# Kernel tuning notes

Hardware: AMD Instinct MI355X
Metric: run time of the kernel (lower is better)

Reference implementation:

```python
import jax, jax.numpy as jnp
import numpy as np

N_NODES = 100000
N_EDGES = 1600000
D_FEAT = 32
EPS = 1e-12  # F.normalize clamp eps


def setup_inputs() -> dict:
    key = jax.random.key(0)
    k1, k2, k3 = jax.random.split(key, 3)
    feat = jax.random.normal(k1, (N_NODES, D_FEAT), dtype=jnp.float32)
    beta = jnp.ones((1,), dtype=jnp.float32)
    src = jax.random.randint(k2, (N_EDGES,), 0, N_NODES, dtype=jnp.int32)
    dst = jax.random.randint(k3, (N_EDGES,), 0, N_NODES, dtype=jnp.int32)
    return {"feat": feat, "beta": beta, "src": src, "dst": dst}


def reference(feat, beta, src, dst):
    N = feat.shape[0]
    # L2-normalize node features (torch.nn.functional.normalize semantics)
    norm = jnp.maximum(jnp.linalg.norm(feat, axis=-1, keepdims=True), EPS)
    norm_h = feat / norm
    # per-edge cosine similarity: u_dot_v
    cos = jnp.sum(norm_h[src] * norm_h[dst], axis=-1)  # [E]
    e = beta[0] * cos
    # edge softmax over incoming edges of each dst node
    m = jax.lax.stop_gradient(jax.ops.segment_max(e, dst, num_segments=N))
    m = jnp.where(jnp.isfinite(m), m, 0.0)  # nodes with no in-edges
    p = jnp.exp(e - m[dst])
    s = jax.ops.segment_sum(p, dst, num_segments=N)
    p = p / s[dst]
    # weighted message aggregation: u_mul_e -> sum
    out = jax.ops.segment_sum(feat[src] * p[:, None], dst, num_segments=N)
    return out
```

## Files before the change

kernel.cpp:

```cpp
#include <hip/hip_runtime.h>
#include <hip/hip_bf16.h>

#define D_FEAT 32
#define BUCKET_SHIFT 7
#define BUCKET_NODES 128
#define MAX_NB 1024
#define CHUNK_E 8192
#define REC_CHUNK 4096

typedef __attribute__((ext_vector_type(8))) unsigned short u16x8;
typedef __attribute__((ext_vector_type(8))) float f32x8;

static __device__ __forceinline__ unsigned short f2bf(float x) {
    unsigned int u = __float_as_uint(x);
    u += 0x7FFFu + ((u >> 16) & 1u);
    return (unsigned short)(u >> 16);
}
static __device__ __forceinline__ float bf2f(unsigned short b) {
    return __uint_as_float((unsigned int)b << 16);
}

__global__ __launch_bounds__(256) void prep_hist_kernel(
    const float* __restrict__ feat,
    unsigned short* __restrict__ nfb,
    float* __restrict__ inv_norm,
    const int* __restrict__ dst,
    int* __restrict__ chunk_hist,
    int n_nodes, int n_edges, int nb, int nchunk) {

    __shared__ int s_h[MAX_NB];
    int bid = blockIdx.x;
    int t = threadIdx.x;

    if (bid < nchunk) {
        for (int i = t; i < MAX_NB; i += 256) s_h[i] = 0;
        __syncthreads();
        int base = bid * CHUNK_E;
        int cnt = min(CHUNK_E, n_edges - base);
        int cnt4 = cnt >> 2;
        const int4* dst4 = reinterpret_cast<const int4*>(dst + base);
        for (int k = t; k < cnt4; k += 256) {
            int4 d4 = dst4[k];
            atomicAdd(&s_h[d4.x >> BUCKET_SHIFT], 1);
            atomicAdd(&s_h[d4.y >> BUCKET_SHIFT], 1);
            atomicAdd(&s_h[d4.z >> BUCKET_SHIFT], 1);
            atomicAdd(&s_h[d4.w >> BUCKET_SHIFT], 1);
        }
        for (int k = (cnt4 << 2) + t; k < cnt; k += 256)
            atomicAdd(&s_h[dst[base + k] >> BUCKET_SHIFT], 1);
        __syncthreads();
        for (int i = t; i < nb; i += 256)
            chunk_hist[(size_t)i * nchunk + bid] = s_h[i];
    } else {
        int g = (bid - nchunk) * 256 + t;
        int node = g >> 3;
        int lane = g & 7;
        if (node >= n_nodes) return;
        float4 v = reinterpret_cast<const float4*>(feat + (size_t)node * D_FEAT)[lane];
        float ss = v.x * v.x + v.y * v.y + v.z * v.z + v.w * v.w;
        #pragma unroll
        for (int m = 4; m; m >>= 1) ss += __shfl_xor(ss, m, 8);
        if (lane == 0) inv_norm[node] = 1.0f / fmaxf(sqrtf(ss), 1e-12f);
        ushort4 b;
        b.x = f2bf(v.x); b.y = f2bf(v.y); b.z = f2bf(v.z); b.w = f2bf(v.w);
        reinterpret_cast<ushort4*>(nfb + (size_t)node * D_FEAT)[lane] = b;
    }
}

__global__ void col_prefix_kernel(int* __restrict__ chunk_hist,
                                  int* __restrict__ total, int nchunk, int nb) {
    int wid  = (blockIdx.x * blockDim.x + threadIdx.x) >> 6;
    int lane = threadIdx.x & 63;
    if (wid >= nb) return;
    int* row = chunk_hist + (size_t)wid * nchunk;
    int run = 0;
    for (int base = 0; base < nchunk; base += 64) {
        int c = base + lane;
        int v = (c < nchunk) ? row[c] : 0;
        int incl = v;
        #pragma unroll
        for (int off = 1; off < 64; off <<= 1) {
            int n = __shfl_up(incl, off, 64);
            if (lane >= off) incl += n;
        }
        if (c < nchunk) row[c] = run + (incl - v);
        run += __shfl(incl, 63, 64);
    }
    if (lane == 0) total[wid] = run;
}

__global__ __launch_bounds__(256) void base_scan_kernel(const int* __restrict__ total,
                                                        int* __restrict__ bucket_base,
                                                        int nb, int n_edges) {
    __shared__ int s_sum[256];
    int t = threadIdx.x;
    int i0 = t * 4;
    int a[4];
    int tsum = 0;
    #pragma unroll
    for (int j = 0; j < 4; ++j) {
        a[j] = (i0 + j < nb) ? total[i0 + j] : 0;
        tsum += a[j];
    }
    s_sum[t] = tsum;
    __syncthreads();
    for (int off = 1; off < 256; off <<= 1) {
        int add = (t >= off) ? s_sum[t - off] : 0;
        __syncthreads();
        s_sum[t] += add;
        __syncthreads();
    }
    int run = s_sum[t] - tsum;
    #pragma unroll
    for (int j = 0; j < 4; ++j) {
        if (i0 + j < nb) bucket_base[i0 + j] = run;
        run += a[j];
    }
    if (t == 0) bucket_base[nb] = n_edges;
}

__global__ __launch_bounds__(256) void scatter_kernel(const int* __restrict__ src,
                                                      const int* __restrict__ dst,
                                                      const int* __restrict__ chunk_hist,
                                                      const int* __restrict__ bucket_base,
                                                      int* __restrict__ recs,
                                                      int n_edges, int nb, int nchunk) {
    __shared__ int s_cur[MAX_NB];
    __shared__ int s_off[MAX_NB + 1];
    __shared__ int s_gbase[MAX_NB];
    __shared__ int s_sum[256];
    __shared__ int s_rec[CHUNK_E];
    __shared__ unsigned short s_b[CHUNK_E];

    int c = blockIdx.x;
    int t = threadIdx.x;
    int base = c * CHUNK_E;
    int cnt = min(CHUNK_E, n_edges - base);
    int cnt4 = cnt >> 2;
    const int4* dst4 = reinterpret_cast<const int4*>(dst + base);
    const int4* src4 = reinterpret_cast<const int4*>(src + base);

    for (int i = t; i < MAX_NB; i += 256) s_cur[i] = 0;
    __syncthreads();
    for (int k = t; k < cnt4; k += 256) {
        int4 d4 = dst4[k];
        atomicAdd(&s_cur[d4.x >> BUCKET_SHIFT], 1);
        atomicAdd(&s_cur[d4.y >> BUCKET_SHIFT], 1);
        atomicAdd(&s_cur[d4.z >> BUCKET_SHIFT], 1);
        atomicAdd(&s_cur[d4.w >> BUCKET_SHIFT], 1);
    }
    for (int k = (cnt4 << 2) + t; k < cnt; k += 256)
        atomicAdd(&s_cur[dst[base + k] >> BUCKET_SHIFT], 1);
    __syncthreads();

    int i0 = t * 4;
    int a[4];
    int tsum = 0;
    #pragma unroll
    for (int j = 0; j < 4; ++j) { a[j] = s_cur[i0 + j]; tsum += a[j]; }
    s_sum[t] = tsum;
    __syncthreads();
    for (int off = 1; off < 256; off <<= 1) {
        int add = (t >= off) ? s_sum[t - off] : 0;
        __syncthreads();
        s_sum[t] += add;
        __syncthreads();
    }
    int run = s_sum[t] - tsum;
    #pragma unroll
    for (int j = 0; j < 4; ++j) { s_off[i0 + j] = run; run += a[j]; }
    if (t == 255) s_off[MAX_NB] = run;
    __syncthreads();
    for (int i = t; i < MAX_NB; i += 256) s_cur[i] = s_off[i];
    for (int i = t; i < nb; i += 256)
        s_gbase[i] = bucket_base[i] + chunk_hist[(size_t)i * nchunk + c];
    __syncthreads();

    for (int k = t; k < cnt4; k += 256) {
        int4 d4 = dst4[k];
        int4 s4 = src4[k];
        #pragma unroll
        for (int j = 0; j < 4; ++j) {
            int d = (j == 0) ? d4.x : (j == 1) ? d4.y : (j == 2) ? d4.z : d4.w;
            int s = (j == 0) ? s4.x : (j == 1) ? s4.y : (j == 2) ? s4.z : s4.w;
            int bb = d >> BUCKET_SHIFT;
            int lpos = atomicAdd(&s_cur[bb], 1);
            s_rec[lpos] = (s << BUCKET_SHIFT) | (d & (BUCKET_NODES - 1));
            s_b[lpos] = (unsigned short)bb;
        }
    }
    for (int k = (cnt4 << 2) + t; k < cnt; k += 256) {
        int d = dst[base + k];
        int s = src[base + k];
        int bb = d >> BUCKET_SHIFT;
        int lpos = atomicAdd(&s_cur[bb], 1);
        s_rec[lpos] = (s << BUCKET_SHIFT) | (d & (BUCKET_NODES - 1));
        s_b[lpos] = (unsigned short)bb;
    }
    __syncthreads();

    for (int i = t; i < cnt; i += 256) {
        int bb = s_b[i];
        recs[s_gbase[bb] + (i - s_off[bb])] = s_rec[i];
    }
}

__global__ __launch_bounds__(512) void bucket_aggregate_kernel(
    const unsigned short* __restrict__ nfb,
    const float* __restrict__ inv_norm,
    const int* __restrict__ bucket_base,
    const int* __restrict__ recs,
    const float* __restrict__ beta,
    float* __restrict__ out, int n_nodes) {

    __shared__ int s_rec[REC_CHUNK];
    __shared__ int s_hist[BUCKET_NODES];
    __shared__ int s_off[BUCKET_NODES + 1];

    int b = blockIdx.x;
    int node0 = b * BUCKET_NODES;
    int start = bucket_base[b];
    int end   = bucket_base[b + 1];
    int t = threadIdx.x;
    int group = t >> 2;
    int lane  = t & 3;
    float bscale = beta[0];

    int myv = node0 + group;
    f32x8 bn;
    f32x8 acc;
    float ssum = 0.f;
    #pragma unroll
    for (int j = 0; j < 8; ++j) { bn[j] = 0.f; acc[j] = 0.f; }
    if (myv < n_nodes) {
        u16x8 braw = reinterpret_cast<const u16x8*>(nfb + (size_t)myv * D_FEAT)[lane];
        float invv = inv_norm[myv];
        #pragma unroll
        for (int j = 0; j < 8; ++j) bn[j] = bf2f(braw[j]) * invv;
    }

    for (int cbase = start; cbase < end; cbase += REC_CHUNK) {
        int cnt = min(REC_CHUNK, end - cbase);

        if (t < BUCKET_NODES) s_hist[t] = 0;
        __syncthreads();
        for (int i = t; i < cnt; i += 512)
            atomicAdd(&s_hist[recs[cbase + i] & (BUCKET_NODES - 1)], 1);
        __syncthreads();

        if (t < 64) {
            int v0 = s_hist[2 * t];
            int v1 = s_hist[2 * t + 1];
            int pair = v0 + v1;
            int incl = pair;
            #pragma unroll
            for (int off = 1; off < 64; off <<= 1) {
                int n = __shfl_up(incl, off, 64);
                if (t >= off) incl += n;
            }
            int excl = incl - pair;
            s_off[2 * t]     = excl;
            s_off[2 * t + 1] = excl + v0;
            s_hist[2 * t]     = excl;
            s_hist[2 * t + 1] = excl + v0;
            if (t == 63) s_off[BUCKET_NODES] = incl;
        }
        __syncthreads();

        for (int i = t; i < cnt; i += 512) {
            int r = recs[cbase + i];
            int pos = atomicAdd(&s_hist[r & (BUCKET_NODES - 1)], 1);
            s_rec[pos] = r;
        }
        __syncthreads();

        {
            int rs = s_off[group];
            int re = s_off[group + 1];

            int u0 = 0; float invu0 = 0.f;
            u16x8 araw0;
            #pragma unroll
            for (int j = 0; j < 8; ++j) araw0[j] = 0;
            if (rs < re) {
                u0 = ((unsigned)s_rec[rs]) >> BUCKET_SHIFT;
                invu0 = inv_norm[u0];
                araw0 = reinterpret_cast<const u16x8*>(nfb + (size_t)u0 * D_FEAT)[lane];
            }
            for (int i = rs; i < re; ++i) {
                int u1 = 0; float invu1 = 0.f;
                u16x8 araw1;
                #pragma unroll
                for (int j = 0; j < 8; ++j) araw1[j] = 0;
                if (i + 1 < re) {
                    u1 = ((unsigned)s_rec[i + 1]) >> BUCKET_SHIFT;
                    invu1 = inv_norm[u1];
                    araw1 = reinterpret_cast<const u16x8*>(nfb + (size_t)u1 * D_FEAT)[lane];
                }
                f32x8 a;
                float d = 0.f;
                #pragma unroll
                for (int j = 0; j < 8; ++j) {
                    a[j] = bf2f(araw0[j]);
                    d = fmaf(a[j], bn[j], d);
                }
                d += __shfl_xor(d, 1, 4);
                d += __shfl_xor(d, 2, 4);
                float pe = __expf(bscale * d * invu0);
                #pragma unroll
                for (int j = 0; j < 8; ++j) acc[j] = fmaf(pe, a[j], acc[j]);
                ssum += pe;
                u0 = u1; invu0 = invu1; araw0 = araw1;
            }
        }
        __syncthreads();
    }

    if (myv < n_nodes) {
        float inv_s = (ssum > 0.f) ? (1.0f / ssum) : 0.0f;
        float* op = out + (size_t)myv * D_FEAT + lane * 8;
        reinterpret_cast<float4*>(op)[0] =
            make_float4(acc[0] * inv_s, acc[1] * inv_s, acc[2] * inv_s, acc[3] * inv_s);
        reinterpret_cast<float4*>(op)[1] =
            make_float4(acc[4] * inv_s, acc[5] * inv_s, acc[6] * inv_s, acc[7] * inv_s);
    }
}

__global__ void prep_kernel(const float* __restrict__ feat,
                            unsigned short* __restrict__ nfb,
                            float* __restrict__ inv_norm, int n_nodes) {
    int g = blockIdx.x * blockDim.x + threadIdx.x;
    int node = g >> 3;
    int lane = g & 7;
    if (node >= n_nodes) return;
    float4 v = reinterpret_cast<const float4*>(feat + (size_t)node * D_FEAT)[lane];
    float ss = v.x * v.x + v.y * v.y + v.z * v.z + v.w * v.w;
    #pragma unroll
    for (int m = 4; m; m >>= 1) ss += __shfl_xor(ss, m, 8);
    if (lane == 0) inv_norm[node] = 1.0f / fmaxf(sqrtf(ss), 1e-12f);
    ushort4 b;
    b.x = f2bf(v.x); b.y = f2bf(v.y); b.z = f2bf(v.z); b.w = f2bf(v.w);
    reinterpret_cast<ushort4*>(nfb + (size_t)node * D_FEAT)[lane] = b;
}

__global__ void link_packed_kernel(const int* __restrict__ src,
                                   const int* __restrict__ dst,
                                   int* __restrict__ head,
                                   int2* __restrict__ rec, int n_edges) {
    int stride = gridDim.x * blockDim.x;
    for (int e = blockIdx.x * blockDim.x + threadIdx.x; e < n_edges; e += stride) {
        int d = dst[e];
        int s = src[e];
        int old = atomicExch(&head[d], e);
        rec[e] = make_int2(old, s);
    }
}

__global__ void fused_chase_bf16_kernel(const unsigned short* __restrict__ nfb,
                                        const float* __restrict__ inv_norm,
                                        const int* __restrict__ head,
                                        const int2* __restrict__ rec,
                                        const float* __restrict__ beta,
                                        float* __restrict__ out, int n_nodes) {
    int g = blockIdx.x * blockDim.x + threadIdx.x;
    int node = g >> 2;
    int lane = g & 3;
    if (node >= n_nodes) return;

    float bscale = beta[0];
    float invv = inv_norm[node];
    u16x8 braw = reinterpret_cast<const u16x8*>(nfb + (size_t)node * D_FEAT)[lane];
    f32x8 bn;
    #pragma unroll
    for (int j = 0; j < 8; ++j) bn[j] = bf2f(braw[j]) * invv;

    f32x8 acc;
    #pragma unroll
    for (int j = 0; j < 8; ++j) acc[j] = 0.f;
    float ssum = 0.f;

    int e = head[node];
    while (e >= 0) {
        int2 r = rec[e];
        int en = r.x, u = r.y;
        float invu = inv_norm[u];
        u16x8 araw = reinterpret_cast<const u16x8*>(nfb + (size_t)u * D_FEAT)[lane];
        f32x8 a;
        float d = 0.f;
        #pragma unroll
        for (int j = 0; j < 8; ++j) {
            a[j] = bf2f(araw[j]);
            d = fmaf(a[j], bn[j], d);
        }
        d += __shfl_xor(d, 1, 4);
        d += __shfl_xor(d, 2, 4);
        float pe = __expf(bscale * d * invu);
        #pragma unroll
        for (int j = 0; j < 8; ++j) acc[j] = fmaf(pe, a[j], acc[j]);
        ssum += pe;
        e = en;
    }

    float inv_s = (ssum > 0.f) ? (1.0f / ssum) : 0.0f;
    float* op = out + (size_t)node * D_FEAT + lane * 8;
    reinterpret_cast<float4*>(op)[0] =
        make_float4(acc[0] * inv_s, acc[1] * inv_s, acc[2] * inv_s, acc[3] * inv_s);
    reinterpret_cast<float4*>(op)[1] =
        make_float4(acc[4] * inv_s, acc[5] * inv_s, acc[6] * inv_s, acc[7] * inv_s);
}

__global__ void node_invnorm_kernel(const float* __restrict__ feat,
                                    float* __restrict__ inv_norm, int n_nodes) {
    int g = blockIdx.x * blockDim.x + threadIdx.x;
    int node = g >> 3;
    int lane = g & 7;
    if (node >= n_nodes) return;
    float4 v = reinterpret_cast<const float4*>(feat + (size_t)node * D_FEAT)[lane];
    float ss = v.x * v.x + v.y * v.y + v.z * v.z + v.w * v.w;
    #pragma unroll
    for (int m = 4; m; m >>= 1) ss += __shfl_xor(ss, m, 8);
    if (lane == 0) inv_norm[node] = 1.0f / fmaxf(sqrtf(ss), 1e-12f);
}

__global__ void edge_p_kernel(const float* __restrict__ feat,
                              const float* __restrict__ inv_norm,
                              const int* __restrict__ src,
                              const int* __restrict__ dst,
                              const float* __restrict__ beta,
                              float* __restrict__ p, float* __restrict__ s,
                              int n_edges) {
    int g = blockIdx.x * blockDim.x + threadIdx.x;
    int e = g >> 3;
    int lane = g & 7;
    if (e >= n_edges) return;
    int u = src[e];
    int v = dst[e];
    float4 a = reinterpret_cast<const float4*>(feat + (size_t)u * D_FEAT)[lane];
    float4 b = reinterpret_cast<const float4*>(feat + (size_t)v * D_FEAT)[lane];
    float d = a.x * b.x;
    d = fmaf(a.y, b.y, d);
    d = fmaf(a.z, b.z, d);
    d = fmaf(a.w, b.w, d);
    #pragma unroll
    for (int m = 4; m; m >>= 1) d += __shfl_xor(d, m, 8);
    if (lane == 0) {
        float pe = __expf(beta[0] * d * inv_norm[u] * inv_norm[v]);
        p[e] = pe;
        atomicAdd(&s[v], pe);
    }
}

__global__ void aggregate_atomic_kernel(const float* __restrict__ feat,
                                        const int* __restrict__ src,
                                        const int* __restrict__ dst,
                                        const float* __restrict__ p,
                                        const float* __restrict__ s,
                                        float* __restrict__ out, int n_edges) {
    int g = blockIdx.x * blockDim.x + threadIdx.x;
    int e = g >> 5;
    int lane = g & 31;
    if (e >= n_edges) return;
    int u = src[e];
    int v = dst[e];
    float w = p[e] / s[v];
    atomicAdd(&out[(size_t)v * D_FEAT + lane], feat[(size_t)u * D_FEAT + lane] * w);
}

extern "C" void kernel_launch(void* const* d_in, const int* in_sizes, int n_in,
                              void* d_out, int out_size, void* d_ws, size_t ws_size,
                              hipStream_t stream) {
    const float* feat = (const float*)d_in[0];
    const float* beta = (const float*)d_in[1];
    const int*   src  = (const int*)d_in[2];
    const int*   dst  = (const int*)d_in[3];
    float* out = (float*)d_out;

    int n_nodes = in_sizes[0] / D_FEAT;
    int n_edges = in_sizes[2];
    int nb = (n_nodes + BUCKET_NODES - 1) / BUCKET_NODES;
    int nchunk = (n_edges + CHUNK_E - 1) / CHUNK_E;

    size_t nfb_bytes = (size_t)n_nodes * D_FEAT * 2;
    size_t need_sort = nfb_bytes +
                       ((size_t)n_nodes + (nb + 1) + MAX_NB +
                        (size_t)nb * nchunk + (size_t)n_edges) * 4;
    size_t need_ll = nfb_bytes + (size_t)n_nodes * 8 + (size_t)n_edges * 8;

    bool sort_ok = (ws_size >= need_sort) && (nb <= MAX_NB) &&
                   (n_nodes <= (1 << 24));

    if (sort_ok) {
        unsigned short* nfb = (unsigned short*)d_ws;
        float* inv_norm   = (float*)((char*)d_ws + nfb_bytes);
        int* bucket_base  = (int*)(inv_norm + n_nodes);
        int* total        = bucket_base + (nb + 1);
        int* chunk_hist   = total + MAX_NB;
        int* recs         = chunk_hist + (size_t)nb * nchunk;

        {
            int prep_blocks = (n_nodes * 8 + 255) / 256;
            prep_hist_kernel<<<nchunk + prep_blocks, 256, 0, stream>>>(
                feat, nfb, inv_norm, dst, chunk_hist, n_nodes, n_edges, nb, nchunk);
        }
        {
            int blocks = (nb + 3) / 4;
            col_prefix_kernel<<<blocks, 256, 0, stream>>>(chunk_hist, total, nchunk, nb);
        }
        base_scan_kernel<<<1, 256, 0, stream>>>(total, bucket_base, nb, n_edges);
        scatter_kernel<<<nchunk, 256, 0, stream>>>(src, dst, chunk_hist, bucket_base,
                                                   recs, n_edges, nb, nchunk);
        bucket_aggregate_kernel<<<nb, 512, 0, stream>>>(
            nfb, inv_norm, bucket_base, recs, beta, out, n_nodes);
    } else if (ws_size >= need_ll) {
        unsigned short* nfb = (unsigned short*)d_ws;
        float* inv_norm = (float*)((char*)d_ws + nfb_bytes);
        int*   head     = (int*)(inv_norm + n_nodes);
        int2*  rec      = (int2*)(head + n_nodes);

        hipMemsetAsync(head, 0xFF, (size_t)n_nodes * sizeof(int), stream);
        {
            int tt = n_nodes * 8;
            prep_kernel<<<(tt + 255) / 256, 256, 0, stream>>>(feat, nfb, inv_norm, n_nodes);
        }
        link_packed_kernel<<<2048, 256, 0, stream>>>(src, dst, head, rec, n_edges);
        {
            int tt = n_nodes * 4;
            fused_chase_bf16_kernel<<<(tt + 255) / 256, 256, 0, stream>>>(
                nfb, inv_norm, head, rec, beta, out, n_nodes);
        }
    } else {
        float* inv_norm = (float*)d_ws;
        float* s_sum    = inv_norm + n_nodes;
        float* p        = s_sum + n_nodes;

        hipMemsetAsync(s_sum, 0, (size_t)n_nodes * sizeof(float), stream);
        hipMemsetAsync(out, 0, (size_t)out_size * sizeof(float), stream);

        {
            int tt = n_nodes * 8;
            node_invnorm_kernel<<<(tt + 255) / 256, 256, 0, stream>>>(feat, inv_norm, n_nodes);
        }
        {
            long long tt = (long long)n_edges * 8;
            edge_p_kernel<<<(int)((tt + 255) / 256), 256, 0, stream>>>(
                feat, inv_norm, src, dst, beta, p, s_sum, n_edges);
        }
        {
            long long tt = (long long)n_edges * 32;
            aggregate_atomic_kernel<<<(int)((tt + 255) / 256), 256, 0, stream>>>(
                feat, src, dst, p, s_sum, out, n_edges);
        }
    }
}
```

Baseline: 73.56 us.

## Split each aggregation bucket across two blocks and two edge streams per node

The aggregate kernel now launches two blocks per 128-node bucket, each owning 64 nodes, and assigns two 4-lane groups per node that walk alternating incoming edges, then combines their partial sums through shared memory. Records are loaded into registers once per chunk instead of being read twice from global memory. The scatter kernel is widened to 512 threads per block. The aim is more parallelism and shorter per-node serial chains in the edge loop. The cost is that each bucket's record list is now read and filtered by two blocks, and there is an extra shared-memory reduction.

```diff
diff --git a/kernel.cpp b/kernel.cpp
--- a/kernel.cpp
+++ b/kernel.cpp
@@ -119,7 +119,7 @@
     if (t == 0) bucket_base[nb] = n_edges;
 }
 
-__global__ __launch_bounds__(256) void scatter_kernel(const int* __restrict__ src,
+__global__ __launch_bounds__(512) void scatter_kernel(const int* __restrict__ src,
                                                       const int* __restrict__ dst,
                                                       const int* __restrict__ chunk_hist,
                                                       const int* __restrict__ bucket_base,
@@ -128,7 +128,7 @@
     __shared__ int s_cur[MAX_NB];
     __shared__ int s_off[MAX_NB + 1];
     __shared__ int s_gbase[MAX_NB];
-    __shared__ int s_sum[256];
+    __shared__ int s_sum[512];
     __shared__ int s_rec[CHUNK_E];
     __shared__ unsigned short s_b[CHUNK_E];
 
@@ -140,43 +140,41 @@
     const int4* dst4 = reinterpret_cast<const int4*>(dst + base);
     const int4* src4 = reinterpret_cast<const int4*>(src + base);
 
-    for (int i = t; i < MAX_NB; i += 256) s_cur[i] = 0;
-    __syncthreads();
-    for (int k = t; k < cnt4; k += 256) {
+    for (int i = t; i < MAX_NB; i += 512) s_cur[i] = 0;
+    __syncthreads();
+    for (int k = t; k < cnt4; k += 512) {
         int4 d4 = dst4[k];
         atomicAdd(&s_cur[d4.x >> BUCKET_SHIFT], 1);
         atomicAdd(&s_cur[d4.y >> BUCKET_SHIFT], 1);
         atomicAdd(&s_cur[d4.z >> BUCKET_SHIFT], 1);
         atomicAdd(&s_cur[d4.w >> BUCKET_SHIFT], 1);
     }
-    for (int k = (cnt4 << 2) + t; k < cnt; k += 256)
+    for (int k = (cnt4 << 2) + t; k < cnt; k += 512)
         atomicAdd(&s_cur[dst[base + k] >> BUCKET_SHIFT], 1);
     __syncthreads();
 
-    int i0 = t * 4;
-    int a[4];
-    int tsum = 0;
-    #pragma unroll
-    for (int j = 0; j < 4; ++j) { a[j] = s_cur[i0 + j]; tsum += a[j]; }
+    int i0 = t * 2;
+    int a0 = s_cur[i0], a1 = s_cur[i0 + 1];
+    int tsum = a0 + a1;
     s_sum[t] = tsum;
     __syncthreads();
-    for (int off = 1; off < 256; off <<= 1) {
+    for (int off = 1; off < 512; off <<= 1) {
         int add = (t >= off) ? s_sum[t - off] : 0;
         __syncthreads();
         s_sum[t] += add;
         __syncthreads();
     }
     int run = s_sum[t] - tsum;
-    #pragma unroll
-    for (int j = 0; j < 4; ++j) { s_off[i0 + j] = run; run += a[j]; }
-    if (t == 255) s_off[MAX_NB] = run;
-    __syncthreads();
-    for (int i = t; i < MAX_NB; i += 256) s_cur[i] = s_off[i];
-    for (int i = t; i < nb; i += 256)
+    s_off[i0] = run;
+    s_off[i0 + 1] = run + a0;
+    if (t == 511) s_off[MAX_NB] = run + tsum;
+    __syncthreads();
+    for (int i = t; i < MAX_NB; i += 512) s_cur[i] = s_off[i];
+    for (int i = t; i < nb; i += 512)
         s_gbase[i] = bucket_base[i] + chunk_hist[(size_t)i * nchunk + c];
     __syncthreads();
 
-    for (int k = t; k < cnt4; k += 256) {
+    for (int k = t; k < cnt4; k += 512) {
         int4 d4 = dst4[k];
         int4 s4 = src4[k];
         #pragma unroll
@@ -189,7 +187,7 @@
             s_b[lpos] = (unsigned short)bb;
         }
     }
-    for (int k = (cnt4 << 2) + t; k < cnt; k += 256) {
+    for (int k = (cnt4 << 2) + t; k < cnt; k += 512) {
         int d = dst[base + k];
         int s = src[base + k];
         int bb = d >> BUCKET_SHIFT;
@@ -199,7 +197,7 @@
     }
     __syncthreads();
 
-    for (int i = t; i < cnt; i += 256) {
+    for (int i = t; i < cnt; i += 512) {
         int bb = s_b[i];
         recs[s_gbase[bb] + (i - s_off[bb])] = s_rec[i];
     }
@@ -214,19 +212,24 @@
     float* __restrict__ out, int n_nodes) {
 
     __shared__ int s_rec[REC_CHUNK];
-    __shared__ int s_hist[BUCKET_NODES];
-    __shared__ int s_off[BUCKET_NODES + 1];
-
-    int b = blockIdx.x;
-    int node0 = b * BUCKET_NODES;
+    __shared__ int s_hist[64];
+    __shared__ int s_off[65];
+    __shared__ float s_part[64][36];
+
+    int blk = blockIdx.x;
+    int b    = blk >> 1;
+    int half = blk & 1;
+    int node0 = b * BUCKET_NODES + half * 64;
     int start = bucket_base[b];
     int end   = bucket_base[b + 1];
     int t = threadIdx.x;
     int group = t >> 2;
     int lane  = t & 3;
+    int nodeLocal = group & 63;
+    int sub = group >> 6;
     float bscale = beta[0];
 
-    int myv = node0 + group;
+    int myv = node0 + nodeLocal;
     f32x8 bn;
     f32x8 acc;
     float ssum = 0.f;
@@ -242,81 +245,103 @@
     for (int cbase = start; cbase < end; cbase += REC_CHUNK) {
         int cnt = min(REC_CHUNK, end - cbase);
 
-        if (t < BUCKET_NODES) s_hist[t] = 0;
-        __syncthreads();
-        for (int i = t; i < cnt; i += 512)
-            atomicAdd(&s_hist[recs[cbase + i] & (BUCKET_NODES - 1)], 1);
+        int r[8];
+        #pragma unroll
+        for (int j = 0; j < 8; ++j) {
+            int k = t + j * 512;
+            r[j] = (k < cnt) ? recs[cbase + k] : -1;
+        }
+
+        if (t < 64) s_hist[t] = 0;
+        __syncthreads();
+        #pragma unroll
+        for (int j = 0; j < 8; ++j)
+            if (r[j] >= 0) {
+                int dl = r[j] & (BUCKET_NODES - 1);
+                if ((dl >> 6) == half) atomicAdd(&s_hist[dl & 63], 1);
+            }
         __syncthreads();
 
         if (t < 64) {
-            int v0 = s_hist[2 * t];
-            int v1 = s_hist[2 * t + 1];
-            int pair = v0 + v1;
-            int incl = pair;
+            int v = s_hist[t];
+            int incl = v;
             #pragma unroll
             for (int off = 1; off < 64; off <<= 1) {
                 int n = __shfl_up(incl, off, 64);
                 if (t >= off) incl += n;
             }
-            int excl = incl - pair;
-            s_off[2 * t]     = excl;
-            s_off[2 * t + 1] = excl + v0;
-            s_hist[2 * t]     = excl;
-            s_hist[2 * t + 1] = excl + v0;
-            if (t == 63) s_off[BUCKET_NODES] = incl;
-        }
-        __syncthreads();
-
-        for (int i = t; i < cnt; i += 512) {
-            int r = recs[cbase + i];
-            int pos = atomicAdd(&s_hist[r & (BUCKET_NODES - 1)], 1);
-            s_rec[pos] = r;
-        }
-        __syncthreads();
-
-        {
-            int rs = s_off[group];
-            int re = s_off[group + 1];
-
-            int u0 = 0; float invu0 = 0.f;
-            u16x8 araw0;
+            s_off[t + 1] = incl;
+            if (t == 0) s_off[0] = 0;
+            s_hist[t] = incl - v;
+        }
+        __syncthreads();
+
+        #pragma unroll
+        for (int j = 0; j < 8; ++j)
+            if (r[j] >= 0) {
+                int dl = r[j] & (BUCKET_NODES - 1);
+                if ((dl >> 6) == half) {
+                    int pos = atomicAdd(&s_hist[dl & 63], 1);
+                    s_rec[pos] = r[j];
+                }
+            }
+        __syncthreads();
+
+        {
+            int rs = s_off[nodeLocal];
+            int re = s_off[nodeLocal + 1];
+            int i = rs + sub;
+
+            int u0 = 0; float inv0 = 0.f;
+            u16x8 raw0;
             #pragma unroll
-            for (int j = 0; j < 8; ++j) araw0[j] = 0;
-            if (rs < re) {
-                u0 = ((unsigned)s_rec[rs]) >> BUCKET_SHIFT;
-                invu0 = inv_norm[u0];
-                araw0 = reinterpret_cast<const u16x8*>(nfb + (size_t)u0 * D_FEAT)[lane];
+            for (int j = 0; j < 8; ++j) raw0[j] = 0;
+            if (i < re) {
+                u0 = ((unsigned)s_rec[i]) >> BUCKET_SHIFT;
+                inv0 = inv_norm[u0];
+                raw0 = reinterpret_cast<const u16x8*>(nfb + (size_t)u0 * D_FEAT)[lane];
             }
-            for (int i = rs; i < re; ++i) {
-                int u1 = 0; float invu1 = 0.f;
-                u16x8 araw1;
+            for (; i < re; i += 2) {
+                int u1 = 0; float inv1 = 0.f;
+                u16x8 raw1;
                 #pragma unroll
-                for (int j = 0; j < 8; ++j) araw1[j] = 0;
-                if (i + 1 < re) {
-                    u1 = ((unsigned)s_rec[i + 1]) >> BUCKET_SHIFT;
-                    invu1 = inv_norm[u1];
-                    araw1 = reinterpret_cast<const u16x8*>(nfb + (size_t)u1 * D_FEAT)[lane];
+                for (int j = 0; j < 8; ++j) raw1[j] = 0;
+                if (i + 2 < re) {
+                    u1 = ((unsigned)s_rec[i + 2]) >> BUCKET_SHIFT;
+                    inv1 = inv_norm[u1];
+                    raw1 = reinterpret_cast<const u16x8*>(nfb + (size_t)u1 * D_FEAT)[lane];
                 }
                 f32x8 a;
                 float d = 0.f;
                 #pragma unroll
                 for (int j = 0; j < 8; ++j) {
-                    a[j] = bf2f(araw0[j]);
+                    a[j] = bf2f(raw0[j]);
                     d = fmaf(a[j], bn[j], d);
                 }
                 d += __shfl_xor(d, 1, 4);
                 d += __shfl_xor(d, 2, 4);
-                float pe = __expf(bscale * d * invu0);
+                float pe = __expf(bscale * d * inv0);
                 #pragma unroll
                 for (int j = 0; j < 8; ++j) acc[j] = fmaf(pe, a[j], acc[j]);
                 ssum += pe;
-                u0 = u1; invu0 = invu1; araw0 = araw1;
+                raw0 = raw1; inv0 = inv1;
             }
         }
         __syncthreads();
     }
 
-    if (myv < n_nodes) {
+    if (sub == 0) {
+        float* p = &s_part[nodeLocal][lane * 8];
+        #pragma unroll
+        for (int j = 0; j < 8; ++j) p[j] = acc[j];
+        if (lane == 0) s_part[nodeLocal][32] = ssum;
+    }
+    __syncthreads();
+    if (sub == 1 && myv < n_nodes) {
+        const float* p = &s_part[nodeLocal][lane * 8];
+        #pragma unroll
+        for (int j = 0; j < 8; ++j) acc[j] += p[j];
+        ssum += s_part[nodeLocal][32];
         float inv_s = (ssum > 0.f) ? (1.0f / ssum) : 0.0f;
         float* op = out + (size_t)myv * D_FEAT + lane * 8;
         reinterpret_cast<float4*>(op)[0] =
@@ -507,9 +532,9 @@
             col_prefix_kernel<<<blocks, 256, 0, stream>>>(chunk_hist, total, nchunk, nb);
         }
         base_scan_kernel<<<1, 256, 0, stream>>>(total, bucket_base, nb, n_edges);
-        scatter_kernel<<<nchunk, 256, 0, stream>>>(src, dst, chunk_hist, bucket_base,
+        scatter_kernel<<<nchunk, 512, 0, stream>>>(src, dst, chunk_hist, bucket_base,
                                                    recs, n_edges, nb, nchunk);
-        bucket_aggregate_kernel<<<nb, 512, 0, stream>>>(
+        bucket_aggregate_kernel<<<nb * 2, 512, 0, stream>>>(
             nfb, inv_norm, bucket_base, recs, beta, out, n_nodes);
     } else if (ws_size >= need_ll) {
         unsigned short* nfb = (unsigned short*)d_ws;
```

Measured after the change: 65.57 us (median of 2 runs). 10.9% less time.
